# Kernel tuning notes

Measured on AMD Instinct MI355X. Metric: run time of the kernel, lower is better.

The kernel has to match this reference:

```python
import jax, jax.numpy as jnp
import numpy as np

N, H, O, E = 32768, 512, 512, 16


def setup_inputs() -> dict:
    key = jax.random.key(0)
    k0, k1, k2 = jax.random.split(key, 3)
    x = jax.random.normal(k0, (N, H), dtype=jnp.float32)
    # gate Linear(H -> E)
    Wg = jax.random.normal(k1, (E, H), dtype=jnp.float32) * (1.0 / np.sqrt(H))
    bg = jnp.zeros((E,), dtype=jnp.float32)
    # expert Linears(H -> O), stacked [E, O, H]
    We = jax.random.normal(k2, (E, O, H), dtype=jnp.float32) * (1.0 / np.sqrt(H))
    be = jnp.zeros((E, O), dtype=jnp.float32)
    return {"x": x, "Wg": Wg, "bg": bg, "We": We, "be": be}


def reference(x, Wg, bg, We, be):
    # gate: softmax over experts, then top-1 (argmax)
    logits = x @ Wg.T + bg                       # [N, E]
    weights = jax.nn.softmax(logits, axis=-1)
    expert_idx = jnp.argmax(weights, axis=-1)    # [N]
    # run every expert on every token, then select the top-1 expert's output.
    # (note: original module does NOT scale output by the gate weight)
    all_out = jnp.einsum('nh,eoh->neo', x, We) + be[None]   # [N, E, O]
    out = jnp.take_along_axis(all_out, expert_idx[:, None, None], axis=1)[:, 0]  # [N, O]
    return out
```

## Files before the change

### kernel.cpp

```cpp
#include <hip/hip_runtime.h>
#include <hip/hip_bf16.h>
#include <stdint.h>

#define NTOK 32768
#define HDIM 512
#define ODIM 512
#define NEXP 16

#define TM 64
#define TN 128
#define BK 32
#define MTILES 64

#define CSTRIDE 32

typedef __bf16 bf16x8 __attribute__((ext_vector_type(8)));
typedef float  floatx4 __attribute__((ext_vector_type(4)));

__device__ __forceinline__ unsigned pk2(unsigned lo, unsigned hi) {
  return (lo >> 16) | (hi & 0xffff0000u);
}

__device__ __forceinline__ bf16x8 asbf8(uint4 u) { bf16x8 v; __builtin_memcpy(&v, &u, 16); return v; }

__device__ __forceinline__ void split3(float4 a, float4 b, uint4* H, uint4* M, uint4* L) {
  float f[8] = {a.x, a.y, a.z, a.w, b.x, b.y, b.z, b.w};
  unsigned h[8], m[8], l[8];
#pragma unroll
  for (int j = 0; j < 8; ++j) {
    union { float F; unsigned U; } u; u.F = f[j];
    h[j] = u.U & 0xffff0000u;
    union { unsigned U; float F; } hv; hv.U = h[j];
    float r1 = f[j] - hv.F;
    union { float F; unsigned U; } r1u; r1u.F = r1;
    m[j] = r1u.U & 0xffff0000u;
    union { unsigned U; float F; } mv; mv.U = m[j];
    float r2 = r1 - mv.F;
    union { float F; unsigned U; } r2u; r2u.F = r2;
    l[j] = r2u.U;
  }
  H->x = pk2(h[0], h[1]); H->y = pk2(h[2], h[3]); H->z = pk2(h[4], h[5]); H->w = pk2(h[6], h[7]);
  M->x = pk2(m[0], m[1]); M->y = pk2(m[2], m[3]); M->z = pk2(m[4], m[5]); M->w = pk2(m[6], m[7]);
  L->x = pk2(l[0], l[1]); L->y = pk2(l[2], l[3]); L->z = pk2(l[4], l[5]); L->w = pk2(l[6], l[7]);
}

#define GLDS16(g, l) __builtin_amdgcn_global_load_lds( \
    (const __attribute__((address_space(1))) unsigned int*)(g), \
    (__attribute__((address_space(3))) unsigned int*)(l), 16, 0, 0)

__global__ __launch_bounds__(256) void cvt_we_kernel(const float* __restrict__ We,
                                                     unsigned short* __restrict__ out) {
  int i = blockIdx.x * 256 + threadIdx.x;
  const float4* src = (const float4*)We;
  float4 a = src[2 * i];
  float4 b = src[2 * i + 1];
  union { float F; unsigned U; } t[8] = {{a.x},{a.y},{a.z},{a.w},{b.x},{b.y},{b.z},{b.w}};
  uint4 o;
  o.x = pk2(t[0].U, t[1].U); o.y = pk2(t[2].U, t[3].U);
  o.z = pk2(t[4].U, t[5].U); o.w = pk2(t[6].U, t[7].U);
  ((uint4*)out)[i] = o;
}

__global__ __launch_bounds__(256, 2) void gate_kernel(const float* __restrict__ x,
                                                      const float* __restrict__ Wg,
                                                      const float* __restrict__ bg,
                                                      int* __restrict__ counts,
                                                      int* __restrict__ buckets,
                                                      unsigned short* __restrict__ xbf) {
  __shared__ __align__(16) unsigned short whf[16][64][8];
  __shared__ __align__(16) unsigned short wmf[16][64][8];
  __shared__ __align__(16) unsigned short wlf[16][64][8];
  __shared__ __align__(16) float red[4][4][16][20];

  int t = threadIdx.x;
  int lane = t & 63;
  int w = t >> 6;
  int tok0 = blockIdx.x * 64;

#pragma unroll
  for (int q = 0; q < 4; ++q) {
    int id = q * 256 + t;
    int s = id >> 6;
    int l = id & 63;
    const float* src = Wg + (size_t)(l & 15) * HDIM + s * 32 + (l >> 4) * 8;
    float4 a = *(const float4*)src;
    float4 b = *(const float4*)(src + 4);
    uint4 H, M, L;
    split3(a, b, &H, &M, &L);
    *(uint4*)&whf[s][l][0] = H;
    *(uint4*)&wmf[s][l][0] = M;
    *(uint4*)&wlf[s][l][0] = L;
  }
  __syncthreads();

  int fr = lane & 15;
  int quad = lane >> 4;
  floatx4 acc[4] = {};

  const float* xbase[4];
#pragma unroll
  for (int mt = 0; mt < 4; ++mt)
    xbase[mt] = x + (size_t)(tok0 + mt * 16 + fr) * HDIM + (w * 4) * 32 + quad * 8;

  float4 xa[4], xb[4];
#pragma unroll
  for (int mt = 0; mt < 4; ++mt) {
    xa[mt] = *(const float4*)(xbase[mt]);
    xb[mt] = *(const float4*)(xbase[mt] + 4);
  }

#pragma unroll
  for (int si = 0; si < 4; ++si) {
    int s = w * 4 + si;
    bf16x8 bh = *(const bf16x8*)&whf[s][lane][0];
    bf16x8 bm = *(const bf16x8*)&wmf[s][lane][0];
    bf16x8 bl = *(const bf16x8*)&wlf[s][lane][0];
    float4 na[4], nb[4];
    if (si < 3) {
#pragma unroll
      for (int mt = 0; mt < 4; ++mt) {
        na[mt] = *(const float4*)(xbase[mt] + (si + 1) * 32);
        nb[mt] = *(const float4*)(xbase[mt] + (si + 1) * 32 + 4);
      }
    }
#pragma unroll
    for (int mt = 0; mt < 4; ++mt) {
      size_t row = tok0 + mt * 16 + fr;
      uint4 H, M, L;
      split3(xa[mt], xb[mt], &H, &M, &L);
      *(uint4*)(xbf + row * HDIM + s * 32 + quad * 8) = H;
      bf16x8 ah = asbf8(H), am = asbf8(M), al = asbf8(L);
      acc[mt] = __builtin_amdgcn_mfma_f32_16x16x32_bf16(ah, bh, acc[mt], 0, 0, 0);
      acc[mt] = __builtin_amdgcn_mfma_f32_16x16x32_bf16(ah, bm, acc[mt], 0, 0, 0);
      acc[mt] = __builtin_amdgcn_mfma_f32_16x16x32_bf16(am, bh, acc[mt], 0, 0, 0);
      acc[mt] = __builtin_amdgcn_mfma_f32_16x16x32_bf16(am, bm, acc[mt], 0, 0, 0);
      acc[mt] = __builtin_amdgcn_mfma_f32_16x16x32_bf16(ah, bl, acc[mt], 0, 0, 0);
      acc[mt] = __builtin_amdgcn_mfma_f32_16x16x32_bf16(al, bh, acc[mt], 0, 0, 0);
      acc[mt] = __builtin_amdgcn_mfma_f32_16x16x32_bf16(am, bl, acc[mt], 0, 0, 0);
      acc[mt] = __builtin_amdgcn_mfma_f32_16x16x32_bf16(al, bm, acc[mt], 0, 0, 0);
    }
    if (si < 3) {
#pragma unroll
      for (int mt = 0; mt < 4; ++mt) { xa[mt] = na[mt]; xb[mt] = nb[mt]; }
    }
  }

#pragma unroll
  for (int mt = 0; mt < 4; ++mt)
#pragma unroll
    for (int i = 0; i < 4; ++i)
      red[w][mt][quad * 4 + i][fr] = acc[mt][i];
  __syncthreads();

  if (t < 64) {
    int tk = t;
    int mt = tk >> 4;
    int r = tk & 15;
    float4 tot4[4];
#pragma unroll
    for (int eq = 0; eq < 4; ++eq) tot4[eq] = *(const float4*)&bg[eq * 4];
#pragma unroll
    for (int ww = 0; ww < 4; ++ww)
#pragma unroll
      for (int eq = 0; eq < 4; ++eq) {
        float4 v = *(const float4*)&red[ww][mt][r][eq * 4];
        tot4[eq].x += v.x; tot4[eq].y += v.y; tot4[eq].z += v.z; tot4[eq].w += v.w;
      }
    float tot[16];
#pragma unroll
    for (int eq = 0; eq < 4; ++eq) {
      tot[eq * 4 + 0] = tot4[eq].x; tot[eq * 4 + 1] = tot4[eq].y;
      tot[eq * 4 + 2] = tot4[eq].z; tot[eq * 4 + 3] = tot4[eq].w;
    }
    float bv = tot[0]; int bi = 0;
#pragma unroll
    for (int e = 1; e < NEXP; ++e) if (tot[e] > bv) { bv = tot[e]; bi = e; }

    int token = tok0 + tk;
    for (int ee = 0; ee < NEXP; ++ee) {
      int e = (ee + blockIdx.x) & 15;
      unsigned long long mask = __ballot(bi == e);
      if (mask) {
        int leader = __builtin_ctzll(mask);
        int base = 0;
        if (lane == leader) base = atomicAdd(&counts[e << 5], (int)__popcll(mask));
        base = __shfl(base, leader, 64);
        if (bi == e) {
          int rank = (int)__popcll(mask & ((1ull << lane) - 1ull));
          buckets[e * NTOK + base + rank] = token;
        }
      }
    }
  }
}

__global__ __launch_bounds__(256, 6) void moe_gemm(const unsigned short* __restrict__ xbf,
                                                   const unsigned short* __restrict__ webf,
                                                   const float* __restrict__ be,
                                                   const int* __restrict__ counts,
                                                   const int* __restrict__ buckets,
                                                   float* __restrict__ out) {
  int e = blockIdx.z;
  int cnt = counts[e << 5];
  int m0 = blockIdx.x * TM;
  if (m0 >= cnt) return;
  int o0 = blockIdx.y * TN;

  __shared__ __align__(16) unsigned short As[2][TM * BK];
  __shared__ __align__(16) unsigned short Bs[2][TN * BK];
  __shared__ int toks[TM];

  int t = threadIdx.x;
  int lane = t & 63;
  int w = t >> 6;

  if (t < TM) {
    int r = m0 + t;
    toks[t] = (r < cnt) ? buckets[e * NTOK + r] : buckets[e * NTOK];
  }
  __syncthreads();

  int pl = lane >> 3;
  int sl = lane & 7;
  int slog = sl ^ pl;
  int rsub = 2 * pl + (slog >> 2);
  int cch = slog & 3;

  const unsigned short* agp = xbf + (size_t)toks[w * 16 + rsub] * HDIM + cch * 8;
  const unsigned short* bgp[2];
#pragma unroll
  for (int j = 0; j < 2; ++j) {
    int row = w * 32 + j * 16 + rsub;
    bgp[j] = webf + ((size_t)e * ODIM + o0 + row) * HDIM + cch * 8;
  }

  int wm = (w & 1) * 32;
  int wn = (w >> 1) * 64;
  int fr = lane & 15;
  int quad = lane >> 4;

  int aoff[2], boff[4];
#pragma unroll
  for (int mt = 0; mt < 2; ++mt) {
    int m = wm + mt * 16 + fr;
    int pr = m >> 1;
    aoff[mt] = pr * 64 + (((((m & 1) << 2) | quad) ^ (pr & 7)) << 3);
  }
#pragma unroll
  for (int nt = 0; nt < 4; ++nt) {
    int n = wn + nt * 16 + fr;
    int pn = n >> 1;
    boff[nt] = pn * 64 + (((((n & 1) << 2) | quad) ^ (pn & 7)) << 3);
  }

  float bias[4];
#pragma unroll
  for (int nt = 0; nt < 4; ++nt)
    bias[nt] = be[e * ODIM + o0 + wn + nt * 16 + fr];

  floatx4 acc[2][4] = {};

  GLDS16(agp, As[0] + w * 512);
#pragma unroll
  for (int j = 0; j < 2; ++j)
    GLDS16(bgp[j], Bs[0] + w * 1024 + j * 512);

  for (int k = 0; k < HDIM / BK; ++k) {
    int p = k & 1;
    asm volatile("s_waitcnt vmcnt(0)" ::: "memory");
    __syncthreads();
    if (k < HDIM / BK - 1) {
      int koff = (k + 1) * BK;
      GLDS16(agp + koff, As[1 - p] + w * 512);
#pragma unroll
      for (int j = 0; j < 2; ++j)
        GLDS16(bgp[j] + koff, Bs[1 - p] + w * 1024 + j * 512);
    }

    bf16x8 af[2], bfr[4];
#pragma unroll
    for (int mt = 0; mt < 2; ++mt)
      af[mt] = *(const bf16x8*)(As[p] + aoff[mt]);
#pragma unroll
    for (int nt = 0; nt < 4; ++nt)
      bfr[nt] = *(const bf16x8*)(Bs[p] + boff[nt]);
#pragma unroll
    for (int mt = 0; mt < 2; ++mt)
#pragma unroll
      for (int nt = 0; nt < 4; ++nt)
        acc[mt][nt] = __builtin_amdgcn_mfma_f32_16x16x32_bf16(af[mt], bfr[nt], acc[mt][nt], 0, 0, 0);
  }

  int rbase = wm + quad * 4;
#pragma unroll
  for (int nt = 0; nt < 4; ++nt) {
    int col = o0 + wn + nt * 16 + fr;
#pragma unroll
    for (int mt = 0; mt < 2; ++mt) {
#pragma unroll
      for (int i = 0; i < 4; ++i) {
        int rl = rbase + mt * 16 + i;
        if (m0 + rl < cnt) {
          out[(size_t)toks[rl] * ODIM + col] = acc[mt][nt][i] + bias[nt];
        }
      }
    }
  }
}

#define WS_BUCKETS 4096
#define WS_XBF (WS_BUCKETS + NEXP * NTOK * 4)
#define WS_WEBF (WS_XBF + NTOK * HDIM * 2)

extern "C" void kernel_launch(void* const* d_in, const int* in_sizes, int n_in,
                              void* d_out, int out_size, void* d_ws, size_t ws_size,
                              hipStream_t stream) {
  const float* x  = (const float*)d_in[0];
  const float* Wg = (const float*)d_in[1];
  const float* bg = (const float*)d_in[2];
  const float* We = (const float*)d_in[3];
  const float* be = (const float*)d_in[4];
  float* out = (float*)d_out;
  char* ws = (char*)d_ws;

  int* counts = (int*)ws;
  int* buckets = (int*)(ws + WS_BUCKETS);
  unsigned short* xbf  = (unsigned short*)(ws + WS_XBF);
  unsigned short* webf = (unsigned short*)(ws + WS_WEBF);

  (void)hipMemsetAsync(counts, 0, NEXP * CSTRIDE * 4, stream);
  cvt_we_kernel<<<NEXP * ODIM * HDIM / 8 / 256, 256, 0, stream>>>(We, webf);
  gate_kernel<<<NTOK / 64, 256, 0, stream>>>(x, Wg, bg, counts, buckets, xbf);
  moe_gemm<<<dim3(MTILES, ODIM / TN, NEXP), 256, 0, stream>>>(xbf, webf, be, counts, buckets, out);
}
```

Baseline: 197.3 us.

## Fuse weight conversion and gate into one launch with 16-token gate blocks

The expert-weight bf16 conversion and the gating kernel are merged into a single launch, where trailing blocks do conversion and leading blocks do gating, removing one kernel launch and letting both run concurrently. Gate blocks now cover 16 tokens instead of 64, and Wg is split directly from global memory per wave instead of being staged through shared memory. This gives more, smaller blocks and allows higher occupancy, but the Wg split work is repeated per block and the ballot/atomic bucketing now runs on 16 lanes only.

```diff
diff --git a/kernel.cpp b/kernel.cpp
--- a/kernel.cpp
+++ b/kernel.cpp
@@ -13,6 +13,9 @@
 #define MTILES 64
 
 #define CSTRIDE 32
+
+#define GATE_BLKS (NTOK / 16)
+#define CVT_BLKS (NEXP * ODIM * HDIM / 8 / 256)
 
 typedef __bf16 bf16x8 __attribute__((ext_vector_type(8)));
 typedef float  floatx4 __attribute__((ext_vector_type(4)));
@@ -48,114 +51,84 @@
     (const __attribute__((address_space(1))) unsigned int*)(g), \
     (__attribute__((address_space(3))) unsigned int*)(l), 16, 0, 0)
 
-__global__ __launch_bounds__(256) void cvt_we_kernel(const float* __restrict__ We,
-                                                     unsigned short* __restrict__ out) {
-  int i = blockIdx.x * 256 + threadIdx.x;
-  const float4* src = (const float4*)We;
-  float4 a = src[2 * i];
-  float4 b = src[2 * i + 1];
-  union { float F; unsigned U; } t[8] = {{a.x},{a.y},{a.z},{a.w},{b.x},{b.y},{b.z},{b.w}};
-  uint4 o;
-  o.x = pk2(t[0].U, t[1].U); o.y = pk2(t[2].U, t[3].U);
-  o.z = pk2(t[4].U, t[5].U); o.w = pk2(t[6].U, t[7].U);
-  ((uint4*)out)[i] = o;
-}
-
-__global__ __launch_bounds__(256, 2) void gate_kernel(const float* __restrict__ x,
-                                                      const float* __restrict__ Wg,
-                                                      const float* __restrict__ bg,
-                                                      int* __restrict__ counts,
-                                                      int* __restrict__ buckets,
-                                                      unsigned short* __restrict__ xbf) {
-  __shared__ __align__(16) unsigned short whf[16][64][8];
-  __shared__ __align__(16) unsigned short wmf[16][64][8];
-  __shared__ __align__(16) unsigned short wlf[16][64][8];
-  __shared__ __align__(16) float red[4][4][16][20];
-
+__global__ __launch_bounds__(256, 4) void fused_prep(const float* __restrict__ x,
+                                                     const float* __restrict__ Wg,
+                                                     const float* __restrict__ bg,
+                                                     const float* __restrict__ We,
+                                                     int* __restrict__ counts,
+                                                     int* __restrict__ buckets,
+                                                     unsigned short* __restrict__ xbf,
+                                                     unsigned short* __restrict__ webf) {
+  __shared__ __align__(16) float red[4][16][20];
+
+  int bid = blockIdx.x;
   int t = threadIdx.x;
+
+  if (bid >= GATE_BLKS) {
+    int i = (bid - GATE_BLKS) * 256 + t;
+    const float4* src = (const float4*)We;
+    float4 a = src[2 * i];
+    float4 b = src[2 * i + 1];
+    union { float F; unsigned U; } u[8] = {{a.x},{a.y},{a.z},{a.w},{b.x},{b.y},{b.z},{b.w}};
+    uint4 o;
+    o.x = pk2(u[0].U, u[1].U); o.y = pk2(u[2].U, u[3].U);
+    o.z = pk2(u[4].U, u[5].U); o.w = pk2(u[6].U, u[7].U);
+    ((uint4*)webf)[i] = o;
+    return;
+  }
+
   int lane = t & 63;
   int w = t >> 6;
-  int tok0 = blockIdx.x * 64;
-
-#pragma unroll
-  for (int q = 0; q < 4; ++q) {
-    int id = q * 256 + t;
-    int s = id >> 6;
-    int l = id & 63;
-    const float* src = Wg + (size_t)(l & 15) * HDIM + s * 32 + (l >> 4) * 8;
-    float4 a = *(const float4*)src;
-    float4 b = *(const float4*)(src + 4);
-    uint4 H, M, L;
-    split3(a, b, &H, &M, &L);
-    *(uint4*)&whf[s][l][0] = H;
-    *(uint4*)&wmf[s][l][0] = M;
-    *(uint4*)&wlf[s][l][0] = L;
-  }
-  __syncthreads();
-
+  int tok0 = bid * 16;
   int fr = lane & 15;
   int quad = lane >> 4;
-  floatx4 acc[4] = {};
-
-  const float* xbase[4];
-#pragma unroll
-  for (int mt = 0; mt < 4; ++mt)
-    xbase[mt] = x + (size_t)(tok0 + mt * 16 + fr) * HDIM + (w * 4) * 32 + quad * 8;
-
-  float4 xa[4], xb[4];
-#pragma unroll
-  for (int mt = 0; mt < 4; ++mt) {
-    xa[mt] = *(const float4*)(xbase[mt]);
-    xb[mt] = *(const float4*)(xbase[mt] + 4);
-  }
+
+  const float* xb0 = x + (size_t)(tok0 + fr) * HDIM + w * 128 + quad * 8;
+  const float* wg0 = Wg + (size_t)fr * HDIM + w * 128 + quad * 8;
+
+  floatx4 acc = {};
+
+  float4 xa = *(const float4*)(xb0);
+  float4 xv = *(const float4*)(xb0 + 4);
 
 #pragma unroll
   for (int si = 0; si < 4; ++si) {
     int s = w * 4 + si;
-    bf16x8 bh = *(const bf16x8*)&whf[s][lane][0];
-    bf16x8 bm = *(const bf16x8*)&wmf[s][lane][0];
-    bf16x8 bl = *(const bf16x8*)&wlf[s][lane][0];
-    float4 na[4], nb[4];
+    float4 wa = *(const float4*)(wg0 + si * 32);
+    float4 wb = *(const float4*)(wg0 + si * 32 + 4);
+    uint4 BH, BM, BL;
+    split3(wa, wb, &BH, &BM, &BL);
+    bf16x8 bh = asbf8(BH), bm = asbf8(BM), bl = asbf8(BL);
+
+    float4 nxa, nxv;
     if (si < 3) {
-#pragma unroll
-      for (int mt = 0; mt < 4; ++mt) {
-        na[mt] = *(const float4*)(xbase[mt] + (si + 1) * 32);
-        nb[mt] = *(const float4*)(xbase[mt] + (si + 1) * 32 + 4);
-      }
-    }
-#pragma unroll
-    for (int mt = 0; mt < 4; ++mt) {
-      size_t row = tok0 + mt * 16 + fr;
-      uint4 H, M, L;
-      split3(xa[mt], xb[mt], &H, &M, &L);
-      *(uint4*)(xbf + row * HDIM + s * 32 + quad * 8) = H;
-      bf16x8 ah = asbf8(H), am = asbf8(M), al = asbf8(L);
-      acc[mt] = __builtin_amdgcn_mfma_f32_16x16x32_bf16(ah, bh, acc[mt], 0, 0, 0);
-      acc[mt] = __builtin_amdgcn_mfma_f32_16x16x32_bf16(ah, bm, acc[mt], 0, 0, 0);
-      acc[mt] = __builtin_amdgcn_mfma_f32_16x16x32_bf16(am, bh, acc[mt], 0, 0, 0);
-      acc[mt] = __builtin_amdgcn_mfma_f32_16x16x32_bf16(am, bm, acc[mt], 0, 0, 0);
-      acc[mt] = __builtin_amdgcn_mfma_f32_16x16x32_bf16(ah, bl, acc[mt], 0, 0, 0);
-      acc[mt] = __builtin_amdgcn_mfma_f32_16x16x32_bf16(al, bh, acc[mt], 0, 0, 0);
-      acc[mt] = __builtin_amdgcn_mfma_f32_16x16x32_bf16(am, bl, acc[mt], 0, 0, 0);
-      acc[mt] = __builtin_amdgcn_mfma_f32_16x16x32_bf16(al, bm, acc[mt], 0, 0, 0);
-    }
-    if (si < 3) {
-#pragma unroll
-      for (int mt = 0; mt < 4; ++mt) { xa[mt] = na[mt]; xb[mt] = nb[mt]; }
-    }
-  }
-
-#pragma unroll
-  for (int mt = 0; mt < 4; ++mt)
-#pragma unroll
-    for (int i = 0; i < 4; ++i)
-      red[w][mt][quad * 4 + i][fr] = acc[mt][i];
+      nxa = *(const float4*)(xb0 + (si + 1) * 32);
+      nxv = *(const float4*)(xb0 + (si + 1) * 32 + 4);
+    }
+
+    uint4 H, M, L;
+    split3(xa, xv, &H, &M, &L);
+    *(uint4*)(xbf + (size_t)(tok0 + fr) * HDIM + s * 32 + quad * 8) = H;
+    bf16x8 ah = asbf8(H), am = asbf8(M), al = asbf8(L);
+    acc = __builtin_amdgcn_mfma_f32_16x16x32_bf16(ah, bh, acc, 0, 0, 0);
+    acc = __builtin_amdgcn_mfma_f32_16x16x32_bf16(ah, bm, acc, 0, 0, 0);
+    acc = __builtin_amdgcn_mfma_f32_16x16x32_bf16(am, bh, acc, 0, 0, 0);
+    acc = __builtin_amdgcn_mfma_f32_16x16x32_bf16(am, bm, acc, 0, 0, 0);
+    acc = __builtin_amdgcn_mfma_f32_16x16x32_bf16(ah, bl, acc, 0, 0, 0);
+    acc = __builtin_amdgcn_mfma_f32_16x16x32_bf16(al, bh, acc, 0, 0, 0);
+    acc = __builtin_amdgcn_mfma_f32_16x16x32_bf16(am, bl, acc, 0, 0, 0);
+    acc = __builtin_amdgcn_mfma_f32_16x16x32_bf16(al, bm, acc, 0, 0, 0);
+
+    if (si < 3) { xa = nxa; xv = nxv; }
+  }
+
+#pragma unroll
+  for (int i = 0; i < 4; ++i)
+    red[w][quad * 4 + i][fr] = acc[i];
   __syncthreads();
 
-  if (t < 64) {
-    int tk = t;
-    int mt = tk >> 4;
-    int r = tk & 15;
+  if (t < 16) {
+    int r = t;
     float4 tot4[4];
 #pragma unroll
     for (int eq = 0; eq < 4; ++eq) tot4[eq] = *(const float4*)&bg[eq * 4];
@@ -163,7 +136,7 @@
     for (int ww = 0; ww < 4; ++ww)
 #pragma unroll
       for (int eq = 0; eq < 4; ++eq) {
-        float4 v = *(const float4*)&red[ww][mt][r][eq * 4];
+        float4 v = *(const float4*)&red[ww][r][eq * 4];
         tot4[eq].x += v.x; tot4[eq].y += v.y; tot4[eq].z += v.z; tot4[eq].w += v.w;
       }
     float tot[16];
@@ -176,9 +149,9 @@
 #pragma unroll
     for (int e = 1; e < NEXP; ++e) if (tot[e] > bv) { bv = tot[e]; bi = e; }
 
-    int token = tok0 + tk;
+    int token = tok0 + r;
     for (int ee = 0; ee < NEXP; ++ee) {
-      int e = (ee + blockIdx.x) & 15;
+      int e = (ee + bid) & 15;
       unsigned long long mask = __ballot(bi == e);
       if (mask) {
         int leader = __builtin_ctzll(mask);
@@ -329,7 +302,6 @@
   unsigned short* webf = (unsigned short*)(ws + WS_WEBF);
 
   (void)hipMemsetAsync(counts, 0, NEXP * CSTRIDE * 4, stream);
-  cvt_we_kernel<<<NEXP * ODIM * HDIM / 8 / 256, 256, 0, stream>>>(We, webf);
-  gate_kernel<<<NTOK / 64, 256, 0, stream>>>(x, Wg, bg, counts, buckets, xbf);
+  fused_prep<<<GATE_BLKS + CVT_BLKS, 256, 0, stream>>>(x, Wg, bg, We, counts, buckets, xbf, webf);
   moe_gemm<<<dim3(MTILES, ODIM / TN, NEXP), 256, 0, stream>>>(xbf, webf, be, counts, buckets, out);
 }
```

After: 189.9 us. 1.04x faster.
